# Performance work log

Hardware: AMD Instinct MI355X
Metric: run time of the kernel (lower is better)

## Reference

```python
import jax, jax.numpy as jnp
import numpy as np

B, T, E, D, H = 32, 2048, 512, 1024, 128

def setup_inputs() -> dict:
    key = jax.random.key(0)
    ks = jax.random.split(key, 8)
    encoder_outs = jax.random.normal(ks[0], (B, T, E), dtype=jnp.float32)
    decoder_state = jax.random.normal(ks[1], (B, D), dtype=jnp.float32)
    # valid lengths in [T//2, T]; mask=True on padded positions
    src_lens = jnp.clip(jax.random.randint(ks[2], (B,), 0, T), T // 2, T).astype(jnp.int32)
    mask = jnp.arange(T)[None, :] >= src_lens[:, None]  # [B,T] bool
    # parameters (nn.Linear style: y = x @ W^T + b; here stored pre-transposed)
    W_enc = jax.random.normal(ks[3], (E, H), dtype=jnp.float32) / np.sqrt(E)
    b_enc = jnp.zeros((H,), dtype=jnp.float32)
    W_dec = jax.random.normal(ks[4], (D, H), dtype=jnp.float32) / np.sqrt(D)  # bias=False
    w_w = jax.random.normal(ks[5], (H, 1), dtype=jnp.float32) / np.sqrt(H)
    w_b = jnp.zeros((1,), dtype=jnp.float32)
    return {"encoder_outs": encoder_outs, "src_lens": src_lens, "decoder_state": decoder_state,
            "mask": mask, "W_enc": W_enc, "b_enc": b_enc, "W_dec": W_dec, "w_w": w_w, "w_b": w_b}

def reference(encoder_outs, src_lens, decoder_state, mask, W_enc, b_enc, W_dec, w_w, w_b):
    # processed_memory = mlp_enc(encoder_outs): [B,T,H]
    processed = jnp.einsum('bte,eh->bth', encoder_outs, W_enc) + b_enc
    # mlp_dec(decoder_state).unsqueeze(1): [B,1,H]
    dec = (decoder_state @ W_dec)[:, None, :]
    # erg = w(tanh(processed + dec)).squeeze(-1): [B,T]
    erg = jnp.einsum('bth,h->bt', jnp.tanh(processed + dec), w_w[:, 0]) + w_b[0]
    erg = jnp.where(mask, -jnp.inf, erg)
    attention_weights = jax.nn.softmax(erg, axis=1)  # [B,T]
    attention_context = jnp.einsum('bte,bt->be', encoder_outs, attention_weights)  # [B,E]
    return attention_context, attention_weights
```

## Files before the change

### kernel.cpp

```cpp
#include <hip/hip_runtime.h>
#include <hip/hip_bf16.h>

#define B 32
#define T 2048
#define E 512
#define D 1024
#define H 128

typedef __attribute__((ext_vector_type(8))) short bf16x8;
typedef __attribute__((ext_vector_type(4))) float f32x4;

static __device__ __forceinline__ short f2b(float f) {
  __hip_bfloat16 h = __float2bfloat16(f);
  return __builtin_bit_cast(short, h);
}

__global__ __launch_bounds__(256) void wet_kernel(
    const float* __restrict__ We, char* __restrict__ WeT) {
  const int id = blockIdx.x * 256 + threadIdx.x;
  const int c = id >> 10;
  const int rem = id & 1023;
  const int h = rem >> 3;
  const int s = rem & 7;
  const int k0 = c * 64 + s * 8;
  bf16x8 v;
#pragma unroll
  for (int j = 0; j < 8; ++j) v[j] = f2b(We[(k0 + j) * H + h]);
  *(bf16x8*)(WeT + c * 16384 + h * 128 + ((s ^ (h & 7)) * 16)) = v;
}

__global__ __launch_bounds__(512) void dec_kernel(
    const float* __restrict__ ds, const float* __restrict__ Wd,
    const float* __restrict__ be, float* __restrict__ dec_ws) {
  const int b = blockIdx.x;
  const int tid = threadIdx.x;
  const int h = tid & 127;
  const int kg = tid >> 7;
  __shared__ float sds[D];
  __shared__ float sred[4][H];
  for (int i = tid; i < D; i += 512) sds[i] = ds[b * D + i];
  __syncthreads();
  float acc = 0.0f;
  const int k0 = kg * 256;
#pragma unroll 8
  for (int k = k0; k < k0 + 256; ++k) acc = fmaf(sds[k], Wd[k * H + h], acc);
  sred[kg][h] = acc;
  __syncthreads();
  if (kg == 0)
    dec_ws[b * H + h] = be[h] + sred[0][h] + sred[1][h] + sred[2][h] + sred[3][h];
}

__global__ __launch_bounds__(256, 3) void erg_mfma_kernel(
    const float* __restrict__ enc, const char* __restrict__ WeT,
    const float* __restrict__ dec_ws, const float* __restrict__ ww,
    const float* __restrict__ wb, float* __restrict__ erg_ws) {
  __shared__ __align__(16) char smem[2][16384];
  const int tid = threadIdx.x;
  const int w = tid >> 6;
  const int lane = tid & 63;
  const int m = lane & 15;
  const int g = lane >> 4;
  const int row0 = blockIdx.x * 64 + w * 16;
  const int b = row0 >> 11;

  f32x4 acc[8];
#pragma unroll
  for (int n = 0; n < 8; ++n) {
    const float d = dec_ws[b * H + n * 16 + m];
    acc[n] = (f32x4){d, d, d, d};
  }

  const float* arow = enc + (size_t)(row0 + m) * E;

  {
    const char* gsrc = WeT + w * 4096 + lane * 16;
    char* ldst = (char*)&smem[0][w * 4096];
#pragma unroll
    for (int i = 0; i < 4; ++i)
      __builtin_amdgcn_global_load_lds(
          (const __attribute__((address_space(1))) void*)(gsrc + i * 1024),
          (__attribute__((address_space(3))) void*)(ldst + i * 1024), 16, 0, 0);
  }
  asm volatile("s_waitcnt vmcnt(0)" ::: "memory");
  __syncthreads();

  for (int c = 0; c < 8; ++c) {
    const int cur = c & 1;
    if (c < 7) {
      const char* gsrc = WeT + (c + 1) * 16384 + w * 4096 + lane * 16;
      char* ldst = (char*)&smem[cur ^ 1][w * 4096];
#pragma unroll
      for (int i = 0; i < 4; ++i)
        __builtin_amdgcn_global_load_lds(
            (const __attribute__((address_space(1))) void*)(gsrc + i * 1024),
            (__attribute__((address_space(3))) void*)(ldst + i * 1024), 16, 0, 0);
    }
    const float* ak = arow + c * 64 + g * 8;
    const float4 a0 = *(const float4*)(ak);
    const float4 a1 = *(const float4*)(ak + 4);
    const float4 a2 = *(const float4*)(ak + 32);
    const float4 a3 = *(const float4*)(ak + 36);
    bf16x8 af0, af1;
    af0[0] = f2b(a0.x); af0[1] = f2b(a0.y); af0[2] = f2b(a0.z); af0[3] = f2b(a0.w);
    af0[4] = f2b(a1.x); af0[5] = f2b(a1.y); af0[6] = f2b(a1.z); af0[7] = f2b(a1.w);
    af1[0] = f2b(a2.x); af1[1] = f2b(a2.y); af1[2] = f2b(a2.z); af1[3] = f2b(a2.w);
    af1[4] = f2b(a3.x); af1[5] = f2b(a3.y); af1[6] = f2b(a3.z); af1[7] = f2b(a3.w);

#pragma unroll
    for (int kk = 0; kk < 2; ++kk) {
      const int slot = (((kk * 4) + g) ^ (lane & 7)) * 16;
      const bf16x8 af = kk ? af1 : af0;
#pragma unroll
      for (int n = 0; n < 8; ++n) {
        const bf16x8 bf =
            *(const bf16x8*)(&smem[cur][(n * 16 + m) * 128 + slot]);
        acc[n] = __builtin_amdgcn_mfma_f32_16x16x32_bf16(af, bf, acc[n], 0, 0, 0);
      }
    }
    asm volatile("s_waitcnt vmcnt(0)" ::: "memory");
    __syncthreads();
  }

  const float wbv = wb[0];
  float wwreg[8];
#pragma unroll
  for (int n = 0; n < 8; ++n) wwreg[n] = ww[n * 16 + m];
#pragma unroll
  for (int j = 0; j < 4; ++j) {
    float gsum = 0.0f;
#pragma unroll
    for (int n = 0; n < 8; ++n) {
      const float x = acc[n][j];
      const float th = 1.0f - 2.0f / (__expf(2.0f * x) + 1.0f);
      gsum = fmaf(wwreg[n], th, gsum);
    }
#pragma unroll
    for (int off = 1; off < 16; off <<= 1) gsum += __shfl_xor(gsum, off, 64);
    if (m == 0) erg_ws[row0 + g * 4 + j] = gsum + wbv;
  }
}

__global__ __launch_bounds__(256) void softmax_kernel(
    const float* __restrict__ erg_ws, const int* __restrict__ src_lens,
    float* __restrict__ wout) {
  const int b = blockIdx.x;
  const int n = src_lens[b];
  const int tid = threadIdx.x;
  const int lane = tid & 63, wid = tid >> 6;
  __shared__ float sm[4];

  float v[T / 256];
  float mx = -1e30f;
#pragma unroll
  for (int r = 0; r < T / 256; ++r) {
    const int t = tid + r * 256;
    const float x = erg_ws[b * T + t];
    v[r] = (t < n) ? x : -1e30f;
    mx = fmaxf(mx, v[r]);
  }
#pragma unroll
  for (int off = 32; off > 0; off >>= 1) mx = fmaxf(mx, __shfl_xor(mx, off, 64));
  if (lane == 0) sm[wid] = mx;
  __syncthreads();
  mx = fmaxf(fmaxf(sm[0], sm[1]), fmaxf(sm[2], sm[3]));
  __syncthreads();

  float s = 0.0f;
#pragma unroll
  for (int r = 0; r < T / 256; ++r) {
    const float e = (v[r] > -1e29f) ? __expf(v[r] - mx) : 0.0f;
    v[r] = e;
    s += e;
  }
#pragma unroll
  for (int off = 32; off > 0; off >>= 1) s += __shfl_xor(s, off, 64);
  if (lane == 0) sm[wid] = s;
  __syncthreads();
  s = sm[0] + sm[1] + sm[2] + sm[3];
  const float inv = 1.0f / s;
#pragma unroll
  for (int r = 0; r < T / 256; ++r) wout[b * T + tid + r * 256] = v[r] * inv;
}

__global__ __launch_bounds__(256) void ctxp_kernel(
    const float* __restrict__ enc, const float* __restrict__ w,
    float* __restrict__ part) {
  const int b = blockIdx.y;
  const int ch = blockIdx.x;
  const int e4 = threadIdx.x & 127;
  const int tp = threadIdx.x >> 7;
  __shared__ float sw[128];
  if (threadIdx.x < 128) sw[threadIdx.x] = w[b * T + ch * 128 + threadIdx.x];
  __syncthreads();
  const float4* ep = (const float4*)(enc + ((size_t)b * T + ch * 128) * E) + e4;
  float4 acc = {0.0f, 0.0f, 0.0f, 0.0f};
#pragma unroll 8
  for (int t = tp; t < 128; t += 2) {
    const float4 e = ep[(size_t)t * (E / 4)];
    const float wv = sw[t];
    acc.x = fmaf(e.x, wv, acc.x);
    acc.y = fmaf(e.y, wv, acc.y);
    acc.z = fmaf(e.z, wv, acc.z);
    acc.w = fmaf(e.w, wv, acc.w);
  }
  *(float4*)(part + ((size_t)(b * 32 + ch * 2 + tp)) * E + e4 * 4) = acc;
}

__global__ __launch_bounds__(128) void ctxr_kernel(
    const float* __restrict__ part, float* __restrict__ ctx) {
  const int b = blockIdx.x;
  const int e4 = threadIdx.x;
  float4 acc = {0.0f, 0.0f, 0.0f, 0.0f};
#pragma unroll
  for (int p = 0; p < 32; ++p) {
    const float4 v = *(const float4*)(part + ((size_t)(b * 32 + p)) * E + e4 * 4);
    acc.x += v.x; acc.y += v.y; acc.z += v.z; acc.w += v.w;
  }
  *(float4*)(ctx + b * E + e4 * 4) = acc;
}

extern "C" void kernel_launch(void* const* d_in, const int* in_sizes, int n_in,
                              void* d_out, int out_size, void* d_ws,
                              size_t ws_size, hipStream_t stream) {
  const float* enc = (const float*)d_in[0];
  const int* src_lens = (const int*)d_in[1];
  const float* ds = (const float*)d_in[2];
  const float* We = (const float*)d_in[4];
  const float* be = (const float*)d_in[5];
  const float* Wd = (const float*)d_in[6];
  const float* ww = (const float*)d_in[7];
  const float* wb = (const float*)d_in[8];

  float* ctx_out = (float*)d_out;
  float* w_out = (float*)d_out + B * E;

  float* ws = (float*)d_ws;
  float* dec_ws = ws;
  float* erg_ws = ws + B * H;
  char* WeT = (char*)(ws + B * H + B * T);
  float* part = ws + B * H + B * T + 32768;

  wet_kernel<<<32, 256, 0, stream>>>(We, WeT);
  dec_kernel<<<B, 512, 0, stream>>>(ds, Wd, be, dec_ws);
  erg_mfma_kernel<<<(B * T) / 64, 256, 0, stream>>>(enc, WeT, dec_ws, ww, wb, erg_ws);
  softmax_kernel<<<B, 256, 0, stream>>>(erg_ws, src_lens, w_out);
  ctxp_kernel<<<dim3(16, B), 256, 0, stream>>>(enc, w_out, part);
  ctxr_kernel<<<B, 128, 0, stream>>>(part, ctx_out);
}
```

Measured before the change: 254.3 us.

## Stage full W_enc in LDS per 1024-thread block and prefetch activations in registers

```diff
diff --git a/kernel.cpp b/kernel.cpp
--- a/kernel.cpp
+++ b/kernel.cpp
@@ -15,53 +15,60 @@
   return __builtin_bit_cast(short, h);
 }
 
-__global__ __launch_bounds__(256) void wet_kernel(
-    const float* __restrict__ We, char* __restrict__ WeT) {
-  const int id = blockIdx.x * 256 + threadIdx.x;
-  const int c = id >> 10;
-  const int rem = id & 1023;
-  const int h = rem >> 3;
-  const int s = rem & 7;
-  const int k0 = c * 64 + s * 8;
-  bf16x8 v;
-#pragma unroll
-  for (int j = 0; j < 8; ++j) v[j] = f2b(We[(k0 + j) * H + h]);
-  *(bf16x8*)(WeT + c * 16384 + h * 128 + ((s ^ (h & 7)) * 16)) = v;
-}
-
-__global__ __launch_bounds__(512) void dec_kernel(
+__global__ __launch_bounds__(512) void prep_kernel(
     const float* __restrict__ ds, const float* __restrict__ Wd,
-    const float* __restrict__ be, float* __restrict__ dec_ws) {
-  const int b = blockIdx.x;
+    const float* __restrict__ be, const float* __restrict__ We,
+    float* __restrict__ dec_ws, char* __restrict__ WeT) {
   const int tid = threadIdx.x;
-  const int h = tid & 127;
-  const int kg = tid >> 7;
-  __shared__ float sds[D];
-  __shared__ float sred[4][H];
-  for (int i = tid; i < D; i += 512) sds[i] = ds[b * D + i];
-  __syncthreads();
-  float acc = 0.0f;
-  const int k0 = kg * 256;
+  if (blockIdx.x < 32) {
+    const int b = blockIdx.x;
+    const int h = tid & 127;
+    const int kg = tid >> 7;
+    __shared__ float sds[D];
+    __shared__ float sred[4][H];
+    for (int i = tid; i < D; i += 512) sds[i] = ds[b * D + i];
+    __syncthreads();
+    float acc = 0.0f;
+    const int k0 = kg * 256;
 #pragma unroll 8
-  for (int k = k0; k < k0 + 256; ++k) acc = fmaf(sds[k], Wd[k * H + h], acc);
-  sred[kg][h] = acc;
-  __syncthreads();
-  if (kg == 0)
-    dec_ws[b * H + h] = be[h] + sred[0][h] + sred[1][h] + sred[2][h] + sred[3][h];
-}
-
-__global__ __launch_bounds__(256, 3) void erg_mfma_kernel(
+    for (int k = k0; k < k0 + 256; ++k) acc = fmaf(sds[k], Wd[k * H + h], acc);
+    sred[kg][h] = acc;
+    __syncthreads();
+    if (kg == 0)
+      dec_ws[b * H + h] = be[h] + sred[0][h] + sred[1][h] + sred[2][h] + sred[3][h];
+  } else {
+    const int id = (blockIdx.x - 32) * 512 + tid;
+    const int c = id >> 10;
+    const int rem = id & 1023;
+    const int h = rem & 127;
+    const int s = rem >> 7;
+    const int k0 = c * 64 + s * 8;
+    bf16x8 v;
+#pragma unroll
+    for (int j = 0; j < 8; ++j) v[j] = f2b(We[(k0 + j) * H + h]);
+    *(bf16x8*)(WeT + c * 16384 + h * 128 + ((s ^ (h & 7)) * 16)) = v;
+  }
+}
+
+__global__ __launch_bounds__(1024, 1) void erg_mfma_kernel(
     const float* __restrict__ enc, const char* __restrict__ WeT,
     const float* __restrict__ dec_ws, const float* __restrict__ ww,
     const float* __restrict__ wb, float* __restrict__ erg_ws) {
-  __shared__ __align__(16) char smem[2][16384];
+  __shared__ __align__(16) char smem[131072];
   const int tid = threadIdx.x;
+  const int lane = tid & 63;
   const int w = tid >> 6;
-  const int lane = tid & 63;
   const int m = lane & 15;
   const int g = lane >> 4;
-  const int row0 = blockIdx.x * 64 + w * 16;
+  const int row0 = blockIdx.x * 256 + w * 16;
   const int b = row0 >> 11;
+
+#pragma unroll
+  for (int j = 0; j < 8; ++j)
+    __builtin_amdgcn_global_load_lds(
+        (const __attribute__((address_space(1))) void*)(WeT + j * 16384 + tid * 16),
+        (__attribute__((address_space(3))) void*)(&smem[j * 16384 + tid * 16]),
+        16, 0, 0);
 
   f32x4 acc[8];
 #pragma unroll
@@ -70,36 +77,26 @@
     acc[n] = (f32x4){d, d, d, d};
   }
 
-  const float* arow = enc + (size_t)(row0 + m) * E;
-
-  {
-    const char* gsrc = WeT + w * 4096 + lane * 16;
-    char* ldst = (char*)&smem[0][w * 4096];
-#pragma unroll
-    for (int i = 0; i < 4; ++i)
-      __builtin_amdgcn_global_load_lds(
-          (const __attribute__((address_space(1))) void*)(gsrc + i * 1024),
-          (__attribute__((address_space(3))) void*)(ldst + i * 1024), 16, 0, 0);
-  }
+  const float* arow = enc + (size_t)(row0 + m) * E + g * 8;
+
+  float4 a0 = *(const float4*)(arow);
+  float4 a1 = *(const float4*)(arow + 4);
+  float4 a2 = *(const float4*)(arow + 32);
+  float4 a3 = *(const float4*)(arow + 36);
+
   asm volatile("s_waitcnt vmcnt(0)" ::: "memory");
   __syncthreads();
 
+#pragma unroll
   for (int c = 0; c < 8; ++c) {
-    const int cur = c & 1;
+    float4 n0, n1, n2, n3;
     if (c < 7) {
-      const char* gsrc = WeT + (c + 1) * 16384 + w * 4096 + lane * 16;
-      char* ldst = (char*)&smem[cur ^ 1][w * 4096];
-#pragma unroll
-      for (int i = 0; i < 4; ++i)
-        __builtin_amdgcn_global_load_lds(
-            (const __attribute__((address_space(1))) void*)(gsrc + i * 1024),
-            (__attribute__((address_space(3))) void*)(ldst + i * 1024), 16, 0, 0);
+      const float* ak = arow + (c + 1) * 64;
+      n0 = *(const float4*)(ak);
+      n1 = *(const float4*)(ak + 4);
+      n2 = *(const float4*)(ak + 32);
+      n3 = *(const float4*)(ak + 36);
     }
-    const float* ak = arow + c * 64 + g * 8;
-    const float4 a0 = *(const float4*)(ak);
-    const float4 a1 = *(const float4*)(ak + 4);
-    const float4 a2 = *(const float4*)(ak + 32);
-    const float4 a3 = *(const float4*)(ak + 36);
     bf16x8 af0, af1;
     af0[0] = f2b(a0.x); af0[1] = f2b(a0.y); af0[2] = f2b(a0.z); af0[3] = f2b(a0.w);
     af0[4] = f2b(a1.x); af0[5] = f2b(a1.y); af0[6] = f2b(a1.z); af0[7] = f2b(a1.w);
@@ -108,17 +105,16 @@
 
 #pragma unroll
     for (int kk = 0; kk < 2; ++kk) {
-      const int slot = (((kk * 4) + g) ^ (lane & 7)) * 16;
+      const int slot = (((kk * 4) + g) ^ (m & 7)) * 16;
       const bf16x8 af = kk ? af1 : af0;
 #pragma unroll
       for (int n = 0; n < 8; ++n) {
         const bf16x8 bf =
-            *(const bf16x8*)(&smem[cur][(n * 16 + m) * 128 + slot]);
+            *(const bf16x8*)(&smem[c * 16384 + (n * 16 + m) * 128 + slot]);
         acc[n] = __builtin_amdgcn_mfma_f32_16x16x32_bf16(af, bf, acc[n], 0, 0, 0);
       }
     }
-    asm volatile("s_waitcnt vmcnt(0)" ::: "memory");
-    __syncthreads();
+    a0 = n0; a1 = n1; a2 = n2; a3 = n3;
   }
 
   const float wbv = wb[0];
@@ -240,9 +236,8 @@
   char* WeT = (char*)(ws + B * H + B * T);
   float* part = ws + B * H + B * T + 32768;
 
-  wet_kernel<<<32, 256, 0, stream>>>(We, WeT);
-  dec_kernel<<<B, 512, 0, stream>>>(ds, Wd, be, dec_ws);
-  erg_mfma_kernel<<<(B * T) / 64, 256, 0, stream>>>(enc, WeT, dec_ws, ww, wb, erg_ws);
+  prep_kernel<<<48, 512, 0, stream>>>(ds, Wd, be, We, dec_ws, WeT);
+  erg_mfma_kernel<<<(B * T) / 256, 1024, 0, stream>>>(enc, WeT, dec_ws, ww, wb, erg_ws);
   softmax_kernel<<<B, 256, 0, stream>>>(erg_ws, src_lens, w_out);
   ctxp_kernel<<<dim3(16, B), 256, 0, stream>>>(enc, w_out, part);
   ctxr_kernel<<<B, 128, 0, stream>>>(part, ctx_out);
```

Result: no change. 257.5 us (+1.3%).
